# Optimization experiments

Hardware: AMD Instinct MI355X
Metric: run time of the kernel (lower is better)

The kernel has to match this reference:

```python
import jax, jax.numpy as jnp
import numpy as np

N_NODES = 50000
N_EDGES = 800000
IN_DIM, HID, N_CLS = 128, 128, 64


def setup_inputs() -> dict:
    key = jax.random.key(0)
    ks = jax.random.split(key, 10)
    x = jax.random.normal(ks[0], (N_NODES, IN_DIM), dtype=jnp.float32)
    src = jax.random.randint(ks[1], (N_EDGES,), 0, N_NODES, dtype=jnp.int32)
    dst = jax.random.randint(ks[2], (N_EDGES,), 0, N_NODES, dtype=jnp.int32)
    def lin(k, fi, fo):
        s = 1.0 / np.sqrt(fi)
        return jax.random.uniform(k, (fi, fo), jnp.float32, -s, s)
    # layer dims: 128->128, 128->128, 128->64 (num_layers=2 -> 3 SAGEConv layers)
    params = {
        'W_self0': lin(ks[3], IN_DIM, HID), 'W_neigh0': lin(ks[4], IN_DIM, HID),
        'b0': jnp.zeros((HID,), jnp.float32),
        'W_self1': lin(ks[5], HID, HID), 'W_neigh1': lin(ks[6], HID, HID),
        'b1': jnp.zeros((HID,), jnp.float32),
        'W_self2': lin(ks[7], HID, N_CLS), 'W_neigh2': lin(ks[8], HID, N_CLS),
        'b2': jnp.zeros((N_CLS,), jnp.float32),
    }
    return {'x': x, 'src': src, 'dst': dst, **params}


def _sage_layer(h, src, dst, W_self, W_neigh, b):
    # mean aggregator: gather source features, segment-sum into dst, divide by in-degree
    msg = h[src]                                                   # [E, d]
    agg = jax.ops.segment_sum(msg, dst, num_segments=N_NODES)      # [N, d]
    deg = jax.ops.segment_sum(jnp.ones((src.shape[0],), h.dtype), dst,
                              num_segments=N_NODES)
    h_neigh = agg / jnp.maximum(deg, 1.0)[:, None]
    return h @ W_self + h_neigh @ W_neigh + b


def reference(x, src, dst, W_self0, W_neigh0, b0, W_self1, W_neigh1, b1,
              W_self2, W_neigh2, b2):
    h = _sage_layer(x, src, dst, W_self0, W_neigh0, b0)
    h = jax.nn.relu(h)
    h = _sage_layer(h, src, dst, W_self1, W_neigh1, b1)
    h = jax.nn.relu(h)
    h = _sage_layer(h, src, dst, W_self2, W_neigh2, b2)
    return h
```

## Files before the change

### kernel.cpp

```cpp
#include <hip/hip_runtime.h>
#include <hip/hip_bf16.h>


#define NFEAT 128
#define SLOTS 64
#define BSH 9
#define BNODES (1 << BSH)
#define MAXBK 100
#define LCAP 64
#define LSH 6
#define MAXTB 256

typedef __attribute__((ext_vector_type(8))) short short8;
typedef __attribute__((ext_vector_type(4))) float floatx4;

__device__ __forceinline__ float bf_lo(unsigned u) { return __uint_as_float(u << 16); }
__device__ __forceinline__ float bf_hi(unsigned u) { return __uint_as_float(u & 0xffff0000u); }
__device__ __forceinline__ ushort f2bf(float f) {
    __hip_bfloat16 h = __float2bfloat16(f);
    return *(ushort*)&h;
}
__device__ __forceinline__ unsigned pack2(float a, float b) {
    return (unsigned)f2bf(a) | ((unsigned)f2bf(b) << 16);
}


__global__ __launch_bounds__(256) void k_p1(
    const int* __restrict__ dst, const int* __restrict__ src,
    unsigned* __restrict__ gbuf, int* __restrict__ lcnt_g,
    unsigned* __restrict__ spill, int* __restrict__ spill_cnt,
    int E, int nbk, int tb, int epb,
    const float* __restrict__ Ws0, const float* __restrict__ Wn0,
    const float* __restrict__ Ws1, const float* __restrict__ Wn1,
    const float* __restrict__ Ws2, const float* __restrict__ Wn2,
    ushort* __restrict__ Wt0, ushort* __restrict__ Wt1, ushort* __restrict__ Wt2) {
    int b = blockIdx.x, t = threadIdx.x;
    if (b < tb) {
        __shared__ unsigned lists[MAXBK * LCAP];
        __shared__ int lcnt[MAXBK];
        for (int i = t; i < MAXBK; i += 256) lcnt[i] = 0;
        __syncthreads();

        int tile0 = b * epb;
        for (int off = t * 4; off < epb; off += 1024) {
            int base = tile0 + off;
            if (base + 4 <= E) {
                int4 d4 = *(const int4*)(dst + base);
                int4 s4 = *(const int4*)(src + base);
                int dd[4] = {d4.x, d4.y, d4.z, d4.w};
                int ss[4] = {s4.x, s4.y, s4.z, s4.w};
#pragma unroll
                for (int j = 0; j < 4; ++j) {
                    int bkt = dd[j] >> BSH;
                    unsigned pk = ((unsigned)ss[j] << 16) | (unsigned)dd[j];
                    int pos = atomicAdd(&lcnt[bkt], 1);
                    if (pos < LCAP) {
                        lists[(bkt << LSH) + pos] = pk;
                    } else {
                        int g = atomicAdd(spill_cnt, 1);
                        spill[g] = pk;
                    }
                }
            } else {
                for (int e = base; e < E && e < base + 4; ++e) {
                    int d = dst[e];
                    int bkt = d >> BSH;
                    unsigned pk = ((unsigned)src[e] << 16) | (unsigned)d;
                    int pos = atomicAdd(&lcnt[bkt], 1);
                    if (pos < LCAP) {
                        lists[(bkt << LSH) + pos] = pk;
                    } else {
                        int g = atomicAdd(spill_cnt, 1);
                        spill[g] = pk;
                    }
                }
            }
        }
        __syncthreads();

        int lane = t & 63, wid = t >> 6;
        for (int bk = wid; bk < nbk; bk += 4) {
            int c = lcnt[bk];
            if (c > LCAP) c = LCAP;
            if (lane == 0) lcnt_g[bk * tb + b] = c;
            unsigned* seg = gbuf + (((size_t)bk * tb + b) << LSH);
            for (int i = lane; i < c; i += 64) seg[i] = lists[(bk << LSH) + i];
        }
    } else {
        int idx = (b - tb) * 256 + t;
        if (idx < 32768) {
            int n = idx >> 8, k = idx & 255;
            Wt0[idx] = f2bf(k < 128 ? Ws0[k * 128 + n] : Wn0[(k - 128) * 128 + n]);
        } else if (idx < 65536) {
            int l = idx - 32768, n = l >> 8, k = l & 255;
            Wt1[l] = f2bf(k < 128 ? Ws1[k * 128 + n] : Wn1[(k - 128) * 128 + n]);
        } else if (idx < 81920) {
            int l = idx - 65536, n = l >> 8, k = l & 255;
            Wt2[l] = f2bf(k < 128 ? Ws2[k * 64 + n] : Wn2[(k - 128) * 64 + n]);
        }
    }
}


__global__ __launch_bounds__(256) void k_p2(
    const unsigned* __restrict__ gbuf, const int* __restrict__ lcnt_g,
    const unsigned* __restrict__ spill, const int* __restrict__ spill_cnt,
    int* __restrict__ deg, ushort* __restrict__ csr, int NN, int nbk, int tb,
    const float* __restrict__ X, ushort* __restrict__ X16, int n2) {
    int b = blockIdx.x, t = threadIdx.x;
    if (b < nbk) {
        __shared__ int cnt[BNODES];
        __shared__ int scnt[MAXTB];
        for (int i = t; i < BNODES; i += 256) cnt[i] = 0;
        for (int i = t; i < tb; i += 256) scnt[i] = lcnt_g[b * tb + i];
        __syncthreads();
        int n0 = b << BSH;
        const unsigned* bp = gbuf + (((size_t)b * tb) << LSH);
        int total = tb << LSH;
        for (int j0 = t * 4; j0 < total; j0 += 1024) {
            int blk = j0 >> LSH;
            int c = scnt[blk];
            int idx0 = j0 & (LCAP - 1);
            uint4 v = *(const uint4*)(bp + j0);
            unsigned pp[4] = {v.x, v.y, v.z, v.w};
#pragma unroll
            for (int k = 0; k < 4; ++k) {
                if (idx0 + k < c) {
                    unsigned p = pp[k];
                    int d = (int)(p & 0xFFFFu);
                    int s = (int)(p >> 16);
                    int r = atomicAdd(&cnt[d - n0], 1);
                    if (r < SLOTS) csr[(d << 6) + r] = (ushort)s;
                }
            }
        }
        int ns = *spill_cnt;
        for (int j = t; j < ns; j += 256) {
            unsigned p = spill[j];
            int d = (int)(p & 0xFFFFu);
            if ((d >> BSH) == b) {
                int s = (int)(p >> 16);
                int r = atomicAdd(&cnt[d - n0], 1);
                if (r < SLOTS) csr[(d << 6) + r] = (ushort)s;
            }
        }
        __syncthreads();
        for (int i = t; i < BNODES; i += 256) {
            int n = n0 + i;
            if (n < NN) deg[n] = cnt[i];
        }
    } else {
        int i = (b - nbk) * 256 + t;
        if (i < n2) {
            float2 v = ((const float2*)X)[i];
            ((unsigned*)X16)[i] = pack2(v.x, v.y);
        }
    }
}


template <int FEAT, int MODE>
__device__ __forceinline__ void agg_body(int vbid, int nb, int t,
    const ushort* __restrict__ H, const int* __restrict__ deg,
    const ushort* __restrict__ csr, void* __restrict__ outp, int NN) {
    constexpr int LPR = FEAT / 8;
    constexpr int EPG = 64 / LPR;
    constexpr int NS = 8;
    int lane = t & 63, wid = t >> 6;
    int sub = lane / LPR, fl = lane % LPR;
    int wstr = nb * 4;
    int node = vbid * 4 + wid;

    int d_cur = 0;
    int s_cur[NS];
    if (node < NN) {
        d_cur = deg[node];
        const ushort* slot = csr + (node << 6);
#pragma unroll
        for (int k = 0; k < NS; ++k) s_cur[k] = slot[k * EPG + sub];
    }

    while (node < NN) {
        int nnode = node + wstr;
        int d_nxt = 0;
        int s_nxt[NS];
        if (nnode < NN) {
            d_nxt = deg[nnode];
            const ushort* slot2 = csr + (nnode << 6);
#pragma unroll
            for (int k = 0; k < NS; ++k) s_nxt[k] = slot2[k * EPG + sub];
        }

        int dd = d_cur;
        int d = (dd < SLOTS) ? dd : SLOTS;
        float acc[8] = {};
        uint4 v[NS];
#pragma unroll
        for (int k = 0; k < NS; ++k) {
            int e = k * EPG + sub;
            v[k] = make_uint4(0, 0, 0, 0);
            if (e < d) v[k] = *(const uint4*)(H + (size_t)s_cur[k] * FEAT + fl * 8);
        }
#pragma unroll
        for (int k = 0; k < NS; ++k) {
            acc[0] += bf_lo(v[k].x); acc[1] += bf_hi(v[k].x);
            acc[2] += bf_lo(v[k].y); acc[3] += bf_hi(v[k].y);
            acc[4] += bf_lo(v[k].z); acc[5] += bf_hi(v[k].z);
            acc[6] += bf_lo(v[k].w); acc[7] += bf_hi(v[k].w);
        }
        if constexpr (NS * EPG < SLOTS) {
            if (d > NS * EPG) {
                const ushort* slot = csr + (node << 6);
                for (int e = NS * EPG + sub; e < d; e += EPG) {
                    int r = slot[e];
                    uint4 vv = *(const uint4*)(H + (size_t)r * FEAT + fl * 8);
                    acc[0] += bf_lo(vv.x); acc[1] += bf_hi(vv.x);
                    acc[2] += bf_lo(vv.y); acc[3] += bf_hi(vv.y);
                    acc[4] += bf_lo(vv.z); acc[5] += bf_hi(vv.z);
                    acc[6] += bf_lo(vv.w); acc[7] += bf_hi(vv.w);
                }
            }
        }
#pragma unroll
        for (int off = LPR; off < 64; off <<= 1)
#pragma unroll
            for (int i = 0; i < 8; ++i) acc[i] += __shfl_xor(acc[i], off, 64);
        if (sub == 0) {
            float inv = (dd > 0) ? 1.0f / (float)dd : 0.0f;
            if constexpr (MODE == 0) {
                unsigned u[4];
#pragma unroll
                for (int i = 0; i < 4; ++i)
                    u[i] = pack2(acc[2 * i] * inv, acc[2 * i + 1] * inv);
                *(uint4*)((ushort*)outp + (size_t)node * FEAT + fl * 8) =
                    make_uint4(u[0], u[1], u[2], u[3]);
            } else {
                float* O = (float*)outp;
                size_t b = (size_t)node * FEAT + fl * 8;
#pragma unroll
                for (int i = 0; i < 8; ++i) O[b + i] += acc[i] * inv;
            }
        }
        node = nnode;
        d_cur = d_nxt;
#pragma unroll
        for (int k = 0; k < NS; ++k) s_cur[k] = s_nxt[k];
    }
}

__global__ __launch_bounds__(256) void k_agg128(
    const ushort* __restrict__ H, const int* __restrict__ deg,
    const ushort* __restrict__ csr, void* __restrict__ outp, int NN) {
    agg_body<128, 0>(blockIdx.x, gridDim.x, threadIdx.x, H, deg, csr, outp, NN);
}

__global__ __launch_bounds__(256) void k_aggacc(
    const ushort* __restrict__ G2, const int* __restrict__ deg,
    const ushort* __restrict__ csr, float* __restrict__ out, int NN) {
    agg_body<64, 2>(blockIdx.x, gridDim.x, threadIdx.x, G2, deg, csr, out, NN);
}


template <int BM, int BN, int NKB, bool SPLIT, bool OUT_BF16, bool FUSE_D7>
__device__ __forceinline__ void gemm_body(int bid, int t,
    const ushort* __restrict__ Hs, const ushort* __restrict__ Ag,
    const ushort* __restrict__ Wt, int ldw, const float* __restrict__ bias,
    void* __restrict__ Cout, int M, int relu,
    const ushort* __restrict__ Wt2, const float* __restrict__ b2,
    ushort* __restrict__ G2, float* __restrict__ outF) {
    constexpr int NW = BN / 64;
    constexpr int NTHR = 2 * NW * 64;
    constexpr int MT = BM / 32;
    constexpr int LDA = 40;
    __shared__ ushort Asl[BM * LDA];
    __shared__ ushort Bsl[BN * LDA];

    int lane = t & 63;
    int wid = t >> 6;
    int wm = wid & 1, wn = wid >> 1;
    int l15 = lane & 15, quad = lane >> 4;
    int m0 = bid * BM;

    floatx4 acc[MT][4] = {};

    for (int kb = 0; kb < NKB; ++kb) {
        const ushort* Asrc;
        int kOff;
        if constexpr (SPLIT) {
            Asrc = (kb < NKB / 2) ? Hs : Ag;
            kOff = (kb & (NKB / 2 - 1)) * 32;
        } else {
            Asrc = Hs;
            kOff = kb * 32;
        }
        __syncthreads();
#pragma unroll
        for (int id = t; id < BM * 4; id += NTHR) {
            int r = id >> 2, p = id & 3;
            uint4 v = make_uint4(0, 0, 0, 0);
            if (m0 + r < M) v = *(const uint4*)(Asrc + (size_t)(m0 + r) * NFEAT + kOff + p * 8);
            *(uint4*)(&Asl[r * LDA + p * 8]) = v;
        }
#pragma unroll
        for (int id = t; id < BN * 4; id += NTHR) {
            int r = id >> 2, p = id & 3;
            uint4 v = *(const uint4*)(Wt + (size_t)r * ldw + kb * 32 + p * 8);
            *(uint4*)(&Bsl[r * LDA + p * 8]) = v;
        }
        __syncthreads();

        short8 a[MT], b[4];
#pragma unroll
        for (int mt = 0; mt < MT; ++mt)
            a[mt] = *(const short8*)(&Asl[(wm * (MT * 16) + mt * 16 + l15) * LDA + quad * 8]);
#pragma unroll
        for (int nt = 0; nt < 4; ++nt)
            b[nt] = *(const short8*)(&Bsl[(wn * 64 + nt * 16 + l15) * LDA + quad * 8]);
#pragma unroll
        for (int mt = 0; mt < MT; ++mt)
#pragma unroll
            for (int nt = 0; nt < 4; ++nt)
                acc[mt][nt] = __builtin_amdgcn_mfma_f32_16x16x32_bf16(a[mt], b[nt], acc[mt][nt], 0, 0, 0);
    }

    if constexpr (!FUSE_D7) {
#pragma unroll
        for (int mt = 0; mt < MT; ++mt) {
            int mbase = m0 + wm * (MT * 16) + mt * 16 + quad * 4;
#pragma unroll
            for (int nt = 0; nt < 4; ++nt) {
                int col = wn * 64 + nt * 16 + l15;
                float bv = bias ? bias[col] : 0.0f;
#pragma unroll
                for (int r = 0; r < 4; ++r) {
                    int m = mbase + r;
                    if (m < M) {
                        float v = acc[mt][nt][r] + bv;
                        if (relu) v = fmaxf(v, 0.f);
                        if constexpr (OUT_BF16) {
                            ((unsigned short*)Cout)[(size_t)m * BN + col] = f2bf(v);
                        } else {
                            ((float*)Cout)[(size_t)m * BN + col] = v;
                        }
                    }
                }
            }
        }
    } else {
        constexpr int LDG = 136;
        __shared__ ushort Hbl[64 * LDG];
#pragma unroll
        for (int mt = 0; mt < MT; ++mt) {
            int rbase = wm * (MT * 16) + mt * 16 + quad * 4;
#pragma unroll
            for (int nt = 0; nt < 4; ++nt) {
                int col = wn * 64 + nt * 16 + l15;
                float bv = bias[col];
#pragma unroll
                for (int r = 0; r < 4; ++r) {
                    float v = acc[mt][nt][r] + bv;
                    v = fmaxf(v, 0.f);
                    Hbl[(rbase + r) * LDG + col] = f2bf(v);
                }
            }
        }

        floatx4 accS[4] = {};
        floatx4 accP[4] = {};
#pragma unroll
        for (int half = 0; half < 2; ++half) {
#pragma unroll
            for (int kb = 0; kb < 4; ++kb) {
                __syncthreads();
#pragma unroll
                for (int id = t; id < 64 * 4; id += NTHR) {
                    int r = id >> 2, p = id & 3;
                    uint4 v = *(const uint4*)(Wt2 + (size_t)r * 256 + half * 128 + kb * 32 + p * 8);
                    *(uint4*)(&Bsl[r * LDA + p * 8]) = v;
                }
                __syncthreads();
                short8 a = *(const short8*)(&Hbl[(wid * 16 + l15) * LDG + kb * 32 + quad * 8]);
#pragma unroll
                for (int nt = 0; nt < 4; ++nt) {
                    short8 b = *(const short8*)(&Bsl[(nt * 16 + l15) * LDA + quad * 8]);
                    if (half == 0)
                        accS[nt] = __builtin_amdgcn_mfma_f32_16x16x32_bf16(a, b, accS[nt], 0, 0, 0);
                    else
                        accP[nt] = __builtin_amdgcn_mfma_f32_16x16x32_bf16(a, b, accP[nt], 0, 0, 0);
                }
            }
        }
#pragma unroll
        for (int nt = 0; nt < 4; ++nt) {
            int col = nt * 16 + l15;
            float bv = b2[col];
#pragma unroll
            for (int r = 0; r < 4; ++r) {
                int m = m0 + wid * 16 + quad * 4 + r;
                if (m < M) {
                    outF[(size_t)m * 64 + col] = accS[nt][r] + bv;
                    G2[(size_t)m * 64 + col] = f2bf(accP[nt][r]);
                }
            }
        }
    }
}

__global__ __launch_bounds__(256) void k_gemm(
    const ushort* __restrict__ Hs, const ushort* __restrict__ Ag,
    const ushort* __restrict__ Wt, const float* __restrict__ bias,
    ushort* __restrict__ Hout, int M) {
    gemm_body<64, 128, 8, true, true, false>(blockIdx.x, threadIdx.x,
        Hs, Ag, Wt, 256, bias, Hout, M, 1, nullptr, nullptr, nullptr, nullptr);
}

__global__ __launch_bounds__(256) void k_gemm1d7(
    const ushort* __restrict__ Hs, const ushort* __restrict__ Ag,
    const ushort* __restrict__ Wt, const float* __restrict__ bias,
    const ushort* __restrict__ Wt2, const float* __restrict__ b2,
    ushort* __restrict__ G2, float* __restrict__ out, int M) {
    gemm_body<64, 128, 8, true, true, true>(blockIdx.x, threadIdx.x,
        Hs, Ag, Wt, 256, bias, nullptr, M, 1, Wt2, b2, G2, out);
}


static inline size_t align_up(size_t x) { return (x + 255) & ~(size_t)255; }

extern "C" void kernel_launch(void* const* d_in, const int* in_sizes, int n_in,
                              void* d_out, int out_size, void* d_ws, size_t ws_size,
                              hipStream_t stream) {
    const float* x   = (const float*)d_in[0];
    const int*   src = (const int*)d_in[1];
    const int*   dst = (const int*)d_in[2];
    const float* Ws0 = (const float*)d_in[3];
    const float* Wn0 = (const float*)d_in[4];
    const float* b0  = (const float*)d_in[5];
    const float* Ws1 = (const float*)d_in[6];
    const float* Wn1 = (const float*)d_in[7];
    const float* b1  = (const float*)d_in[8];
    const float* Ws2 = (const float*)d_in[9];
    const float* Wn2 = (const float*)d_in[10];
    const float* b2  = (const float*)d_in[11];
    float* out = (float*)d_out;

    const int NN = in_sizes[0] / NFEAT;
    const int E  = in_sizes[1];

    char* w = (char*)d_ws;
    ushort* X16  = (ushort*)w; w += align_up((size_t)NN * NFEAT * 2);
    ushort* Ha   = (ushort*)w; w += align_up((size_t)NN * NFEAT * 2);
    ushort* Hb   = (ushort*)w; w += align_up((size_t)NN * NFEAT * 2);
    ushort* AGG  = (ushort*)w; w += align_up((size_t)NN * NFEAT * 2);
    ushort* Wt0  = (ushort*)w; w += align_up((size_t)128 * 256 * 2);
    ushort* Wt1  = (ushort*)w; w += align_up((size_t)128 * 256 * 2);
    ushort* Wt2  = (ushort*)w; w += align_up((size_t)64 * 256 * 2);
    int* deg     = (int*)w;    w += align_up((size_t)NN * 4);
    ushort* csr  = (ushort*)w; w += align_up((size_t)NN * SLOTS * 2);

    int epb = 4096;
    int tb = (E + epb - 1) / epb;
    if (tb > MAXTB) { epb = ((E + MAXTB - 1) / MAXTB + 1023) & ~(size_t)1023; tb = (E + epb - 1) / epb; }
    const int nbk = (NN + BNODES - 1) >> BSH;

    unsigned* gbuf   = (unsigned*)Ha;
    int* lcnt_g      = (int*)Hb;
    int* spill_cnt   = lcnt_g + nbk * tb;
    unsigned* spill  = (unsigned*)AGG;
    ushort* G2       = X16;

    hipMemsetAsync(spill_cnt, 0, 4, stream);

    const int n2   = NN * NFEAT / 2;
    const int cvtb = (n2 + 255) / 256;
    const int wb   = (81920 + 255) / 256;
    const int gm   = (NN + 63) / 64;
    const int agb  = 2048;

    k_p1<<<tb + wb, 256, 0, stream>>>(
        dst, src, gbuf, lcnt_g, spill, spill_cnt, E, nbk, tb, epb,
        Ws0, Wn0, Ws1, Wn1, Ws2, Wn2, Wt0, Wt1, Wt2);

    k_p2<<<nbk + cvtb, 256, 0, stream>>>(
        gbuf, lcnt_g, spill, spill_cnt, deg, csr, NN, nbk, tb, x, X16, n2);

    k_agg128<<<agb, 256, 0, stream>>>(X16, deg, csr, AGG, NN);
    k_gemm<<<gm, 256, 0, stream>>>(X16, AGG, Wt0, b0, Ha, NN);

    k_agg128<<<agb, 256, 0, stream>>>(Ha, deg, csr, AGG, NN);
    k_gemm1d7<<<gm, 256, 0, stream>>>(Ha, AGG, Wt1, b1, Wt2, b2, G2, out, NN);

    k_aggacc<<<agb, 256, 0, stream>>>(G2, deg, csr, out, NN);
}
```

Baseline: 233.8 us.

## Store node features in 32-column chunk-major layout for cache-friendly aggregation

Features for X16, AGG, Ha and G2 are now stored as separate 32-column chunks, each a contiguous [N,32] array. The aggregation kernels assign each block group to one chunk, so the gathered rows come from a smaller working set that fits better in L2/MALL. Each lane fetch is now 16 bytes of a 64-byte row segment rather than part of a 256-byte row, and the per-node CSR index loads are repeated once per chunk. The X conversion moves from k_p2 into k_p1, and the GEMMs read and write the chunked layout. The old path for nodes with more than 32 neighbours is dropped, since 4x16 slots now cover all 64.

After: 343.1 us. 1.47x slower.

```diff
diff --git a/kernel.cpp b/kernel.cpp
--- a/kernel.cpp
+++ b/kernel.cpp
@@ -30,10 +30,12 @@
     unsigned* __restrict__ gbuf, int* __restrict__ lcnt_g,
     unsigned* __restrict__ spill, int* __restrict__ spill_cnt,
     int E, int nbk, int tb, int epb,
+    const float* __restrict__ X, ushort* __restrict__ X16, int n2, int NN,
     const float* __restrict__ Ws0, const float* __restrict__ Wn0,
     const float* __restrict__ Ws1, const float* __restrict__ Wn1,
     const float* __restrict__ Ws2, const float* __restrict__ Wn2,
-    ushort* __restrict__ Wt0, ushort* __restrict__ Wt1, ushort* __restrict__ Wt2) {
+    ushort* __restrict__ Wt0, ushort* __restrict__ Wt1, ushort* __restrict__ Wt2,
+    int cvtb) {
     int b = blockIdx.x, t = threadIdx.x;
     if (b < tb) {
         __shared__ unsigned lists[MAXBK * LCAP];
@@ -86,8 +88,15 @@
             unsigned* seg = gbuf + (((size_t)bk * tb + b) << LSH);
             for (int i = lane; i < c; i += 64) seg[i] = lists[(bk << LSH) + i];
         }
+    } else if (b < tb + cvtb) {
+        int i = (b - tb) * 256 + t;
+        if (i < n2) {
+            float2 v = ((const float2*)X)[i];
+            int n = i >> 6, c = (i & 63) >> 4, f2 = i & 15;
+            ((unsigned*)(X16 + ((size_t)c * NN + n) * 32))[f2] = pack2(v.x, v.y);
+        }
     } else {
-        int idx = (b - tb) * 256 + t;
+        int idx = (b - tb - cvtb) * 256 + t;
         if (idx < 32768) {
             int n = idx >> 8, k = idx & 255;
             Wt0[idx] = f2bf(k < 128 ? Ws0[k * 128 + n] : Wn0[(k - 128) * 128 + n]);
@@ -105,124 +114,104 @@
 __global__ __launch_bounds__(256) void k_p2(
     const unsigned* __restrict__ gbuf, const int* __restrict__ lcnt_g,
     const unsigned* __restrict__ spill, const int* __restrict__ spill_cnt,
-    int* __restrict__ deg, ushort* __restrict__ csr, int NN, int nbk, int tb,
-    const float* __restrict__ X, ushort* __restrict__ X16, int n2) {
+    int* __restrict__ deg, ushort* __restrict__ csr, int NN, int nbk, int tb) {
     int b = blockIdx.x, t = threadIdx.x;
-    if (b < nbk) {
-        __shared__ int cnt[BNODES];
-        __shared__ int scnt[MAXTB];
-        for (int i = t; i < BNODES; i += 256) cnt[i] = 0;
-        for (int i = t; i < tb; i += 256) scnt[i] = lcnt_g[b * tb + i];
-        __syncthreads();
-        int n0 = b << BSH;
-        const unsigned* bp = gbuf + (((size_t)b * tb) << LSH);
-        int total = tb << LSH;
-        for (int j0 = t * 4; j0 < total; j0 += 1024) {
-            int blk = j0 >> LSH;
-            int c = scnt[blk];
-            int idx0 = j0 & (LCAP - 1);
-            uint4 v = *(const uint4*)(bp + j0);
-            unsigned pp[4] = {v.x, v.y, v.z, v.w};
-#pragma unroll
-            for (int k = 0; k < 4; ++k) {
-                if (idx0 + k < c) {
-                    unsigned p = pp[k];
-                    int d = (int)(p & 0xFFFFu);
-                    int s = (int)(p >> 16);
-                    int r = atomicAdd(&cnt[d - n0], 1);
-                    if (r < SLOTS) csr[(d << 6) + r] = (ushort)s;
-                }
-            }
-        }
-        int ns = *spill_cnt;
-        for (int j = t; j < ns; j += 256) {
-            unsigned p = spill[j];
-            int d = (int)(p & 0xFFFFu);
-            if ((d >> BSH) == b) {
+    __shared__ int cnt[BNODES];
+    __shared__ int scnt[MAXTB];
+    for (int i = t; i < BNODES; i += 256) cnt[i] = 0;
+    for (int i = t; i < tb; i += 256) scnt[i] = lcnt_g[b * tb + i];
+    __syncthreads();
+    int n0 = b << BSH;
+    const unsigned* bp = gbuf + (((size_t)b * tb) << LSH);
+    int total = tb << LSH;
+    for (int j0 = t * 4; j0 < total; j0 += 1024) {
+        int blk = j0 >> LSH;
+        int c = scnt[blk];
+        int idx0 = j0 & (LCAP - 1);
+        uint4 v = *(const uint4*)(bp + j0);
+        unsigned pp[4] = {v.x, v.y, v.z, v.w};
+#pragma unroll
+        for (int k = 0; k < 4; ++k) {
+            if (idx0 + k < c) {
+                unsigned p = pp[k];
+                int d = (int)(p & 0xFFFFu);
                 int s = (int)(p >> 16);
                 int r = atomicAdd(&cnt[d - n0], 1);
                 if (r < SLOTS) csr[(d << 6) + r] = (ushort)s;
             }
         }
-        __syncthreads();
-        for (int i = t; i < BNODES; i += 256) {
-            int n = n0 + i;
-            if (n < NN) deg[n] = cnt[i];
-        }
-    } else {
-        int i = (b - nbk) * 256 + t;
-        if (i < n2) {
-            float2 v = ((const float2*)X)[i];
-            ((unsigned*)X16)[i] = pack2(v.x, v.y);
-        }
-    }
-}
-
-
-template <int FEAT, int MODE>
-__device__ __forceinline__ void agg_body(int vbid, int nb, int t,
+    }
+    int ns = *spill_cnt;
+    for (int j = t; j < ns; j += 256) {
+        unsigned p = spill[j];
+        int d = (int)(p & 0xFFFFu);
+        if ((d >> BSH) == b) {
+            int s = (int)(p >> 16);
+            int r = atomicAdd(&cnt[d - n0], 1);
+            if (r < SLOTS) csr[(d << 6) + r] = (ushort)s;
+        }
+    }
+    __syncthreads();
+    for (int i = t; i < BNODES; i += 256) {
+        int n = n0 + i;
+        if (n < NN) deg[n] = cnt[i];
+    }
+}
+
+
+template <int NCH, int MODE>
+__device__ __forceinline__ void aggc_body(int bid, int nb, int t,
     const ushort* __restrict__ H, const int* __restrict__ deg,
     const ushort* __restrict__ csr, void* __restrict__ outp, int NN) {
-    constexpr int LPR = FEAT / 8;
-    constexpr int EPG = 64 / LPR;
-    constexpr int NS = 8;
+    constexpr int XPC = 8 / NCH;
     int lane = t & 63, wid = t >> 6;
-    int sub = lane / LPR, fl = lane % LPR;
-    int wstr = nb * 4;
-    int node = vbid * 4 + wid;
+    int sub = lane >> 2, fl = lane & 3;
+    int x = bid & 7, g = bid >> 3;
+    int chunk = x / XPC, sb = x % XPC;
+    int NB = (nb >> 3) * XPC;
+    int node = (g * XPC + sb) * 4 + wid;
+    int wstr = NB * 4;
+    const ushort* Hc = H + (size_t)chunk * NN * 32;
 
     int d_cur = 0;
-    int s_cur[NS];
+    int s_cur[4];
     if (node < NN) {
         d_cur = deg[node];
-        const ushort* slot = csr + (node << 6);
-#pragma unroll
-        for (int k = 0; k < NS; ++k) s_cur[k] = slot[k * EPG + sub];
+        const ushort* sl = csr + (node << 6);
+#pragma unroll
+        for (int k = 0; k < 4; ++k) s_cur[k] = sl[k * 16 + sub];
     }
 
     while (node < NN) {
         int nnode = node + wstr;
         int d_nxt = 0;
-        int s_nxt[NS];
+        int s_nxt[4];
         if (nnode < NN) {
             d_nxt = deg[nnode];
-            const ushort* slot2 = csr + (nnode << 6);
-#pragma unroll
-            for (int k = 0; k < NS; ++k) s_nxt[k] = slot2[k * EPG + sub];
+            const ushort* sl = csr + (nnode << 6);
+#pragma unroll
+            for (int k = 0; k < 4; ++k) s_nxt[k] = sl[k * 16 + sub];
         }
 
         int dd = d_cur;
         int d = (dd < SLOTS) ? dd : SLOTS;
         float acc[8] = {};
-        uint4 v[NS];
-#pragma unroll
-        for (int k = 0; k < NS; ++k) {
-            int e = k * EPG + sub;
+        uint4 v[4];
+#pragma unroll
+        for (int k = 0; k < 4; ++k) {
             v[k] = make_uint4(0, 0, 0, 0);
-            if (e < d) v[k] = *(const uint4*)(H + (size_t)s_cur[k] * FEAT + fl * 8);
-        }
-#pragma unroll
-        for (int k = 0; k < NS; ++k) {
+            if (k * 16 + sub < d)
+                v[k] = *(const uint4*)(Hc + (size_t)s_cur[k] * 32 + fl * 8);
+        }
+#pragma unroll
+        for (int k = 0; k < 4; ++k) {
             acc[0] += bf_lo(v[k].x); acc[1] += bf_hi(v[k].x);
             acc[2] += bf_lo(v[k].y); acc[3] += bf_hi(v[k].y);
             acc[4] += bf_lo(v[k].z); acc[5] += bf_hi(v[k].z);
             acc[6] += bf_lo(v[k].w); acc[7] += bf_hi(v[k].w);
         }
-        if constexpr (NS * EPG < SLOTS) {
-            if (d > NS * EPG) {
-                const ushort* slot = csr + (node << 6);
-                for (int e = NS * EPG + sub; e < d; e += EPG) {
-                    int r = slot[e];
-                    uint4 vv = *(const uint4*)(H + (size_t)r * FEAT + fl * 8);
-                    acc[0] += bf_lo(vv.x); acc[1] += bf_hi(vv.x);
-                    acc[2] += bf_lo(vv.y); acc[3] += bf_hi(vv.y);
-                    acc[4] += bf_lo(vv.z); acc[5] += bf_hi(vv.z);
-                    acc[6] += bf_lo(vv.w); acc[7] += bf_hi(vv.w);
-                }
-            }
-        }
-#pragma unroll
-        for (int off = LPR; off < 64; off <<= 1)
+#pragma unroll
+        for (int off = 4; off < 64; off <<= 1)
 #pragma unroll
             for (int i = 0; i < 8; ++i) acc[i] += __shfl_xor(acc[i], off, 64);
         if (sub == 0) {
@@ -232,92 +221,82 @@
 #pragma unroll
                 for (int i = 0; i < 4; ++i)
                     u[i] = pack2(acc[2 * i] * inv, acc[2 * i + 1] * inv);
-                *(uint4*)((ushort*)outp + (size_t)node * FEAT + fl * 8) =
+                *(uint4*)((ushort*)outp + ((size_t)chunk * NN + node) * 32 + fl * 8) =
                     make_uint4(u[0], u[1], u[2], u[3]);
             } else {
                 float* O = (float*)outp;
-                size_t b = (size_t)node * FEAT + fl * 8;
-#pragma unroll
-                for (int i = 0; i < 8; ++i) O[b + i] += acc[i] * inv;
+                size_t base = (size_t)node * 64 + chunk * 32 + fl * 8;
+#pragma unroll
+                for (int i = 0; i < 8; ++i) O[base + i] += acc[i] * inv;
             }
         }
         node = nnode;
         d_cur = d_nxt;
 #pragma unroll
-        for (int k = 0; k < NS; ++k) s_cur[k] = s_nxt[k];
-    }
-}
-
-__global__ __launch_bounds__(256) void k_agg128(
+        for (int k = 0; k < 4; ++k) s_cur[k] = s_nxt[k];
+    }
+}
+
+__global__ __launch_bounds__(256) void k_aggc128(
     const ushort* __restrict__ H, const int* __restrict__ deg,
     const ushort* __restrict__ csr, void* __restrict__ outp, int NN) {
-    agg_body<128, 0>(blockIdx.x, gridDim.x, threadIdx.x, H, deg, csr, outp, NN);
-}
-
-__global__ __launch_bounds__(256) void k_aggacc(
+    aggc_body<4, 0>(blockIdx.x, gridDim.x, threadIdx.x, H, deg, csr, outp, NN);
+}
+
+__global__ __launch_bounds__(256) void k_aggaccc(
     const ushort* __restrict__ G2, const int* __restrict__ deg,
     const ushort* __restrict__ csr, float* __restrict__ out, int NN) {
-    agg_body<64, 2>(blockIdx.x, gridDim.x, threadIdx.x, G2, deg, csr, out, NN);
-}
-
-
-template <int BM, int BN, int NKB, bool SPLIT, bool OUT_BF16, bool FUSE_D7>
+    aggc_body<2, 2>(blockIdx.x, gridDim.x, threadIdx.x, G2, deg, csr, out, NN);
+}
+
+
+template <bool FUSE_D7>
 __device__ __forceinline__ void gemm_body(int bid, int t,
     const ushort* __restrict__ Hs, const ushort* __restrict__ Ag,
-    const ushort* __restrict__ Wt, int ldw, const float* __restrict__ bias,
-    void* __restrict__ Cout, int M, int relu,
+    const ushort* __restrict__ Wt, const float* __restrict__ bias,
+    ushort* __restrict__ HoutC, int M, int NN,
     const ushort* __restrict__ Wt2, const float* __restrict__ b2,
     ushort* __restrict__ G2, float* __restrict__ outF) {
-    constexpr int NW = BN / 64;
-    constexpr int NTHR = 2 * NW * 64;
-    constexpr int MT = BM / 32;
     constexpr int LDA = 40;
-    __shared__ ushort Asl[BM * LDA];
-    __shared__ ushort Bsl[BN * LDA];
+    __shared__ ushort Asl[64 * LDA];
+    __shared__ ushort Bsl[128 * LDA];
 
     int lane = t & 63;
     int wid = t >> 6;
     int wm = wid & 1, wn = wid >> 1;
     int l15 = lane & 15, quad = lane >> 4;
-    int m0 = bid * BM;
-
-    floatx4 acc[MT][4] = {};
-
-    for (int kb = 0; kb < NKB; ++kb) {
-        const ushort* Asrc;
-        int kOff;
-        if constexpr (SPLIT) {
-            Asrc = (kb < NKB / 2) ? Hs : Ag;
-            kOff = (kb & (NKB / 2 - 1)) * 32;
-        } else {
-            Asrc = Hs;
-            kOff = kb * 32;
-        }
+    int m0 = bid * 64;
+
+    floatx4 acc[2][4] = {};
+
+    for (int kb = 0; kb < 8; ++kb) {
+        const ushort* Asrc = (kb < 4) ? Hs : Ag;
+        const ushort* Ac = Asrc + (size_t)(kb & 3) * NN * 32;
         __syncthreads();
 #pragma unroll
-        for (int id = t; id < BM * 4; id += NTHR) {
+        for (int id = t; id < 64 * 4; id += 256) {
             int r = id >> 2, p = id & 3;
             uint4 v = make_uint4(0, 0, 0, 0);
-            if (m0 + r < M) v = *(const uint4*)(Asrc + (size_t)(m0 + r) * NFEAT + kOff + p * 8);
+            if (m0 + r < M) v = *(const uint4*)(Ac + (size_t)(m0 + r) * 32 + p * 8);
             *(uint4*)(&Asl[r * LDA + p * 8]) = v;
         }
 #pragma unroll
-        for (int id = t; id < BN * 4; id += NTHR) {
+        for (int id = t; id < 128 * 4; id += 256) {
             int r = id >> 2, p = id & 3;
-            uint4 v = *(const uint4*)(Wt + (size_t)r * ldw + kb * 32 + p * 8);
+            uint4 v = *(const uint4*)(Wt + (size_t)r * 256 + kb * 32 + p * 8);
             *(uint4*)(&Bsl[r * LDA + p * 8]) = v;
         }
         __syncthreads();
 
-        short8 a[MT], b[4];
-#pragma unroll
-        for (int mt = 0; mt < MT; ++mt)
-            a[mt] = *(const short8*)(&Asl[(wm * (MT * 16) + mt * 16 + l15) * LDA + quad * 8]);
+        short8 a[2], b[4];
+#pragma unroll
+        for (int mt = 0; mt < 2; ++mt)
+            a[mt] = *(const short8*)(&Asl[(wm * 32 + mt * 16 + l15) * LDA + quad * 8]);
 #pragma unroll
         for (int nt = 0; nt < 4; ++nt)
             b[nt] = *(const short8*)(&Bsl[(wn * 64 + nt * 16 + l15) * LDA + quad * 8]);
 #pragma unroll
-        for (int mt = 0; mt < MT; ++mt)
+        for (int mt = 0; mt < 2; ++mt)
 #pragma unroll
             for (int nt = 0; nt < 4; ++nt)
                 acc[mt][nt] = __builtin_amdgcn_mfma_f32_16x16x32_bf16(a[mt], b[nt], acc[mt][nt], 0, 0, 0);
@@ -325,23 +304,20 @@
 
     if constexpr (!FUSE_D7) {
 #pragma unroll
-        for (int mt = 0; mt < MT; ++mt) {
-            int mbase = m0 + wm * (MT * 16) + mt * 16 + quad * 4;
+        for (int mt = 0; mt < 2; ++mt) {
+            int mbase = m0 + wm * 32 + mt * 16 + quad * 4;
 #pragma unroll
             for (int nt = 0; nt < 4; ++nt) {
                 int col = wn * 64 + nt * 16 + l15;
-                float bv = bias ? bias[col] : 0.0f;
+                float bv = bias[col];
+                ushort* dst = HoutC + (size_t)(col >> 5) * NN * 32 + (col & 31);
 #pragma unroll
                 for (int r = 0; r < 4; ++r) {
                     int m = mbase + r;
                     if (m < M) {
                         float v = acc[mt][nt][r] + bv;
-                        if (relu) v = fmaxf(v, 0.f);
-                        if constexpr (OUT_BF16) {
-                            ((unsigned short*)Cout)[(size_t)m * BN + col] = f2bf(v);
-                        } else {
-                            ((float*)Cout)[(size_t)m * BN + col] = v;
-                        }
+                        v = fmaxf(v, 0.f);
+                        dst[(size_t)m * 32] = f2bf(v);
                     }
                 }
             }
@@ -350,8 +326,8 @@
         constexpr int LDG = 136;
         __shared__ ushort Hbl[64 * LDG];
 #pragma unroll
-        for (int mt = 0; mt < MT; ++mt) {
-            int rbase = wm * (MT * 16) + mt * 16 + quad * 4;
+        for (int mt = 0; mt < 2; ++mt) {
+            int rbase = wm * 32 + mt * 16 + quad * 4;
 #pragma unroll
             for (int nt = 0; nt < 4; ++nt) {
                 int col = wn * 64 + nt * 16 + l15;
@@ -373,7 +349,7 @@
             for (int kb = 0; kb < 4; ++kb) {
                 __syncthreads();
 #pragma unroll
-                for (int id = t; id < 64 * 4; id += NTHR) {
+                for (int id = t; id < 64 * 4; id += 256) {
                     int r = id >> 2, p = id & 3;
                     uint4 v = *(const uint4*)(Wt2 + (size_t)r * 256 + half * 128 + kb * 32 + p * 8);
                     *(uint4*)(&Bsl[r * LDA + p * 8]) = v;
@@ -394,33 +370,34 @@
         for (int nt = 0; nt < 4; ++nt) {
             int col = nt * 16 + l15;
             float bv = b2[col];
+            ushort* g2d = G2 + (size_t)(col >> 5) * NN * 32 + (col & 31);
 #pragma unroll
             for (int r = 0; r < 4; ++r) {
                 int m = m0 + wid * 16 + quad * 4 + r;
                 if (m < M) {
                     outF[(size_t)m * 64 + col] = accS[nt][r] + bv;
-                    G2[(size_t)m * 64 + col] = f2bf(accP[nt][r]);
-                }
-            }
-        }
-    }
-}
-
-__global__ __launch_bounds__(256) void k_gemm(
+                    g2d[(size_t)m * 32] = f2bf(accP[nt][r]);
+                }
+            }
+        }
+    }
+}
+
+__global__ __launch_bounds__(256) void k_gemm0(
     const ushort* __restrict__ Hs, const ushort* __restrict__ Ag,
     const ushort* __restrict__ Wt, const float* __restrict__ bias,
-    ushort* __restrict__ Hout, int M) {
-    gemm_body<64, 128, 8, true, true, false>(blockIdx.x, threadIdx.x,
-        Hs, Ag, Wt, 256, bias, Hout, M, 1, nullptr, nullptr, nullptr, nullptr);
+    ushort* __restrict__ HoutC, int M, int NN) {
+    gemm_body<false>(blockIdx.x, threadIdx.x, Hs, Ag, Wt, bias, HoutC, M, NN,
+                     nullptr, nullptr, nullptr, nullptr);
 }
 
 __global__ __launch_bounds__(256) void k_gemm1d7(
     const ushort* __restrict__ Hs, const ushort* __restrict__ Ag,
     const ushort* __restrict__ Wt, const float* __restrict__ bias,
     const ushort* __restrict__ Wt2, const float* __restrict__ b2,
-    ushort* __restrict__ G2, float* __restrict__ out, int M) {
-    gemm_body<64, 128, 8, true, true, true>(blockIdx.x, threadIdx.x,
-        Hs, Ag, Wt, 256, bias, nullptr, M, 1, Wt2, b2, G2, out);
+    ushort* __restrict__ G2, float* __restrict__ out, int M, int NN) {
+    gemm_body<true>(blockIdx.x, threadIdx.x, Hs, Ag, Wt, bias, nullptr, M, NN,
+                    Wt2, b2, G2, out);
 }
 
 
@@ -476,18 +453,19 @@
     const int gm   = (NN + 63) / 64;
     const int agb  = 2048;
 
-    k_p1<<<tb + wb, 256, 0, stream>>>(
+    k_p1<<<tb + cvtb + wb, 256, 0, stream>>>(
         dst, src, gbuf, lcnt_g, spill, spill_cnt, E, nbk, tb, epb,
-        Ws0, Wn0, Ws1, Wn1, Ws2, Wn2, Wt0, Wt1, Wt2);
-
-    k_p2<<<nbk + cvtb, 256, 0, stream>>>(
-        gbuf, lcnt_g, spill, spill_cnt, deg, csr, NN, nbk, tb, x, X16, n2);
-
-    k_agg128<<<agb, 256, 0, stream>>>(X16, deg, csr, AGG, NN);
-    k_gemm<<<gm, 256, 0, stream>>>(X16, AGG, Wt0, b0, Ha, NN);
-
-    k_agg128<<<agb, 256, 0, stream>>>(Ha, deg, csr, AGG, NN);
-    k_gemm1d7<<<gm, 256, 0, stream>>>(Ha, AGG, Wt1, b1, Wt2, b2, G2, out, NN);
-
-    k_aggacc<<<agb, 256, 0, stream>>>(G2, deg, csr, out, NN);
-}
+        x, X16, n2, NN,
+        Ws0, Wn0, Ws1, Wn1, Ws2, Wn2, Wt0, Wt1, Wt2, cvtb);
+
+    k_p2<<<nbk, 256, 0, stream>>>(
+        gbuf, lcnt_g, spill, spill_cnt, deg, csr, NN, nbk, tb);
+
+    k_aggc128<<<agb, 256, 0, stream>>>(X16, deg, csr, AGG, NN);
+    k_gemm0<<<gm, 256, 0, stream>>>(X16, AGG, Wt0, b0, Ha, NN, NN);
+
+    k_aggc128<<<agb, 256, 0, stream>>>(Ha, deg, csr, AGG, NN);
+    k_gemm1d7<<<gm, 256, 0, stream>>>(Ha, AGG, Wt1, b1, Wt2, b2, G2, out, NN, NN);
+
+    k_aggaccc<<<agb, 256, 0, stream>>>(G2, deg, csr, out, NN);
+}
```
